# Optimization experiments

Measured on AMD Instinct MI355X. Metric: run time of the kernel, lower is better.

The kernel has to match this reference:

```python
import jax, jax.numpy as jnp
import numpy as np

GAMMA = 2.0  # args.gamma
B, C, H, W = 8, 21, 512, 512


def setup_inputs() -> dict:
    key = jax.random.key(0)
    k1, k2 = jax.random.split(key)
    pred = jax.random.normal(k1, (B, C, H, W), dtype=jnp.float32)
    # one-hot target built from random per-pixel class labels
    labels = jax.random.randint(k2, (B, H, W), 0, C)
    target = jax.nn.one_hot(labels, C, dtype=jnp.float32)  # [B,H,W,C]
    target = jnp.transpose(target, (0, 3, 1, 2))  # [B,C,H,W]
    return {"pred": pred, "target": target}


def reference(pred, target) -> jnp.ndarray:
    b, c, h, w = pred.shape
    logits = jax.nn.log_softmax(pred, axis=1)  # [B,C,H,W]
    lo = jnp.transpose(logits, (0, 2, 3, 1)).reshape(-1, c)  # [N,C]
    tg = jnp.transpose(target, (0, 2, 3, 1)).reshape(-1, c)  # [N,C]
    n = lo.shape[0]
    beta = (n - 1.0) / n
    # per-pixel focal term summed over channels: sum_j (1-p_j)^gamma * log p_j * t_j
    row_val = jnp.sum((1.0 - jnp.exp(lo)) ** GAMMA * lo * tg, axis=1)  # [N]
    mask = (tg == 1).astype(lo.dtype)  # [N,C] class membership mask
    n_c = jnp.sum(mask, axis=0)  # [C] pixels per class
    class_sum = jnp.einsum('nc,n->c', mask, row_val)  # [C] masked reductions
    w = (1.0 - beta) / (1.0 - jnp.power(jnp.float32(beta), n_c) + 1e-6)  # [C]
    return -jnp.sum(w * class_sum) / n
```

## Files before the change

kernel.cpp:

```cpp
#include <hip/hip_runtime.h>

#define CCH    21
#define HWSZ   (512*512)
#define HW4    (HWSZ/4)
#define NPIX   (8*HWSZ)
#define BLKT   256
#define NBLK   (NPIX/4/BLKT)
#define CB     7
#define NB     3

#define WAIT_VM(n) __builtin_amdgcn_s_waitcnt(0x0F70 | (n))

typedef float vfloat4 __attribute__((ext_vector_type(4)));

__device__ __forceinline__ void stage16(const float* g, vfloat4* l) {
    __builtin_amdgcn_global_load_lds(
        (const __attribute__((address_space(1))) unsigned int*)g,
        (__attribute__((address_space(3))) unsigned int*)l, 16, 0, 0);
}

__global__ __launch_bounds__(BLKT) void cb_focal_partial(
    const float* __restrict__ pred, const float* __restrict__ targ,
    float* __restrict__ gsum, float* __restrict__ gcnt)
{
    __shared__ vfloat4 tbuf[2][CB][BLKT];
    __shared__ float ls_sum[CCH];
    __shared__ float ls_cnt[CCH];
    if (threadIdx.x < CCH) { ls_sum[threadIdx.x] = 0.f; ls_cnt[threadIdx.x] = 0.f; }
    __syncthreads();

    const int tid = blockIdx.x * BLKT + threadIdx.x;
    const int b   = tid >> 16;
    const int hw4 = tid & (HW4 - 1);
    const float* pp = pred + (size_t)b * CCH * HWSZ + (size_t)hw4 * 4;
    const float* tp = targ + (size_t)b * CCH * HWSZ + (size_t)hw4 * 4;
    const int wv = threadIdx.x & 192;

    float s0 = 0.f, s1 = 0.f, s2 = 0.f, s3 = 0.f;
    float vy0 = 0.f, vy1 = 0.f, vy2 = 0.f, vy3 = 0.f;
    float ey0 = 1.f, ey1 = 1.f, ey2 = 1.f, ey3 = 1.f;
    int   y0 = 0, y1 = 0, y2 = 0, y3 = 0;

    vfloat4 v[2][CB];

    #pragma unroll
    for (int j = 0; j < CB; ++j)
        stage16(tp + (size_t)j * HWSZ, &tbuf[0][j][wv]);
    #pragma unroll
    for (int j = 0; j < CB; ++j)
        v[0][j] = __builtin_nontemporal_load((const vfloat4*)(pp + (size_t)j * HWSZ));
    __builtin_amdgcn_sched_barrier(0);

    #pragma unroll
    for (int kk = 0; kk < NB; ++kk) {
        if (kk + 1 < NB) {
            #pragma unroll
            for (int j = 0; j < CB; ++j)
                stage16(tp + (size_t)((kk + 1) * CB + j) * HWSZ,
                        &tbuf[(kk + 1) & 1][j][wv]);
            #pragma unroll
            for (int j = 0; j < CB; ++j)
                v[(kk + 1) & 1][j] = __builtin_nontemporal_load(
                    (const vfloat4*)(pp + (size_t)((kk + 1) * CB + j) * HWSZ));
            __builtin_amdgcn_sched_barrier(0);
            WAIT_VM(14);
        } else {
            __builtin_amdgcn_sched_barrier(0);
            WAIT_VM(0);
        }
        __builtin_amdgcn_sched_barrier(0);

        #pragma unroll
        for (int j = 0; j < CB; ++j) {
            const vfloat4 pv = v[kk & 1][j];
            const vfloat4 t  = tbuf[kk & 1][j][threadIdx.x];
            const int c = kk * CB + j;
            const float e0 = __expf(pv.x), e1 = __expf(pv.y),
                        e2 = __expf(pv.z), e3 = __expf(pv.w);
            s0 += e0; s1 += e1; s2 += e2; s3 += e3;
            const bool h0 = t.x > 0.5f, h1 = t.y > 0.5f,
                       h2 = t.z > 0.5f, h3 = t.w > 0.5f;
            y0 = h0 ? c : y0;  vy0 = h0 ? pv.x : vy0;  ey0 = h0 ? e0 : ey0;
            y1 = h1 ? c : y1;  vy1 = h1 ? pv.y : vy1;  ey1 = h1 ? e1 : ey1;
            y2 = h2 ? c : y2;  vy2 = h2 ? pv.z : vy2;  ey2 = h2 ? e2 : ey2;
            y3 = h3 ? c : y3;  vy3 = h3 ? pv.w : vy3;  ey3 = h3 ? e3 : ey3;
        }
    }

    {
        const float l0 = vy0 - __logf(s0), p0 = ey0 / s0, o0 = 1.f - p0;
        const float l1 = vy1 - __logf(s1), p1 = ey1 / s1, o1 = 1.f - p1;
        const float l2 = vy2 - __logf(s2), p2 = ey2 / s2, o2 = 1.f - p2;
        const float l3 = vy3 - __logf(s3), p3 = ey3 / s3, o3 = 1.f - p3;
        atomicAdd(&ls_sum[y0], o0 * o0 * l0);  atomicAdd(&ls_cnt[y0], 1.f);
        atomicAdd(&ls_sum[y1], o1 * o1 * l1);  atomicAdd(&ls_cnt[y1], 1.f);
        atomicAdd(&ls_sum[y2], o2 * o2 * l2);  atomicAdd(&ls_cnt[y2], 1.f);
        atomicAdd(&ls_sum[y3], o3 * o3 * l3);  atomicAdd(&ls_cnt[y3], 1.f);
    }
    __syncthreads();
    if (threadIdx.x < CCH) {
        atomicAdd(&gsum[threadIdx.x], ls_sum[threadIdx.x]);
        atomicAdd(&gcnt[threadIdx.x], ls_cnt[threadIdx.x]);
    }
}

__global__ void cb_focal_final(const float* __restrict__ gsum,
                               const float* __restrict__ gcnt,
                               float* __restrict__ out)
{
    const int lane = threadIdx.x;
    double term = 0.0;
    if (lane < CCH) {
        const double n    = (double)NPIX;
        const double beta = (n - 1.0) / n;
        const double w = (1.0 - beta) / (1.0 - pow(beta, (double)gcnt[lane]) + 1e-6);
        term = w * (double)gsum[lane];
    }
    for (int off = 32; off; off >>= 1) term += __shfl_down(term, off, 64);
    if (lane == 0) out[0] = (float)(-term / (double)NPIX);
}

extern "C" void kernel_launch(void* const* d_in, const int* in_sizes, int n_in,
                              void* d_out, int out_size, void* d_ws, size_t ws_size,
                              hipStream_t stream) {
    const float* pred = (const float*)d_in[0];
    const float* targ = (const float*)d_in[1];
    float* out  = (float*)d_out;
    float* gsum = (float*)d_ws;
    float* gcnt = gsum + CCH;

    (void)hipMemsetAsync(gsum, 0, 2 * CCH * sizeof(float), stream);
    cb_focal_partial<<<NBLK, BLKT, 0, stream>>>(pred, targ, gsum, gcnt);
    cb_focal_final<<<1, 64, 0, stream>>>(gsum, gcnt, out);
}
```

Before: 346.5 us.

## Replace LDS-staged double buffer with per-channel register prefetch ring

Drops the global_load_lds staging of the one-hot target and the 7-channel double-buffered blocks. Both pred and target now load straight into registers through a 4-deep rolling prefetch ring, with explicit vmcnt waits per channel. This frees shared memory and cuts register pressure, which can raise occupancy. In exchange there are fewer bytes in flight per thread, the hand-counted waitcnt values are fragile, and the nontemporal hint on pred loads is removed.

```diff
diff --git a/kernel.cpp b/kernel.cpp
--- a/kernel.cpp
+++ b/kernel.cpp
@@ -6,24 +6,16 @@
 #define NPIX   (8*HWSZ)
 #define BLKT   256
 #define NBLK   (NPIX/4/BLKT)
-#define CB     7
-#define NB     3
+#define PF     4
 
 #define WAIT_VM(n) __builtin_amdgcn_s_waitcnt(0x0F70 | (n))
 
 typedef float vfloat4 __attribute__((ext_vector_type(4)));
 
-__device__ __forceinline__ void stage16(const float* g, vfloat4* l) {
-    __builtin_amdgcn_global_load_lds(
-        (const __attribute__((address_space(1))) unsigned int*)g,
-        (__attribute__((address_space(3))) unsigned int*)l, 16, 0, 0);
-}
-
 __global__ __launch_bounds__(BLKT) void cb_focal_partial(
     const float* __restrict__ pred, const float* __restrict__ targ,
     float* __restrict__ gsum, float* __restrict__ gcnt)
 {
-    __shared__ vfloat4 tbuf[2][CB][BLKT];
     __shared__ float ls_sum[CCH];
     __shared__ float ls_cnt[CCH];
     if (threadIdx.x < CCH) { ls_sum[threadIdx.x] = 0.f; ls_cnt[threadIdx.x] = 0.f; }
@@ -34,57 +26,47 @@
     const int hw4 = tid & (HW4 - 1);
     const float* pp = pred + (size_t)b * CCH * HWSZ + (size_t)hw4 * 4;
     const float* tp = targ + (size_t)b * CCH * HWSZ + (size_t)hw4 * 4;
-    const int wv = threadIdx.x & 192;
 
     float s0 = 0.f, s1 = 0.f, s2 = 0.f, s3 = 0.f;
     float vy0 = 0.f, vy1 = 0.f, vy2 = 0.f, vy3 = 0.f;
     float ey0 = 1.f, ey1 = 1.f, ey2 = 1.f, ey3 = 1.f;
     int   y0 = 0, y1 = 0, y2 = 0, y3 = 0;
 
-    vfloat4 v[2][CB];
+    vfloat4 pv[PF], tv[PF];
 
     #pragma unroll
-    for (int j = 0; j < CB; ++j)
-        stage16(tp + (size_t)j * HWSZ, &tbuf[0][j][wv]);
-    #pragma unroll
-    for (int j = 0; j < CB; ++j)
-        v[0][j] = __builtin_nontemporal_load((const vfloat4*)(pp + (size_t)j * HWSZ));
-    __builtin_amdgcn_sched_barrier(0);
+    for (int c = 0; c < PF; ++c) {
+        pv[c] = *(const vfloat4*)(pp + (size_t)c * HWSZ);
+        tv[c] = *(const vfloat4*)(tp + (size_t)c * HWSZ);
+        __builtin_amdgcn_sched_barrier(0);
+    }
 
     #pragma unroll
-    for (int kk = 0; kk < NB; ++kk) {
-        if (kk + 1 < NB) {
-            #pragma unroll
-            for (int j = 0; j < CB; ++j)
-                stage16(tp + (size_t)((kk + 1) * CB + j) * HWSZ,
-                        &tbuf[(kk + 1) & 1][j][wv]);
-            #pragma unroll
-            for (int j = 0; j < CB; ++j)
-                v[(kk + 1) & 1][j] = __builtin_nontemporal_load(
-                    (const vfloat4*)(pp + (size_t)((kk + 1) * CB + j) * HWSZ));
-            __builtin_amdgcn_sched_barrier(0);
-            WAIT_VM(14);
-        } else {
-            __builtin_amdgcn_sched_barrier(0);
-            WAIT_VM(0);
+    for (int c = 0; c < CCH; ++c) {
+        if      (c <= CCH - 4) { WAIT_VM(6); }
+        else if (c == CCH - 3) { WAIT_VM(4); }
+        else if (c == CCH - 2) { WAIT_VM(2); }
+        else                   { WAIT_VM(0); }
+        __builtin_amdgcn_sched_barrier(0);
+
+        const vfloat4 p = pv[c % PF];
+        const vfloat4 t = tv[c % PF];
+
+        if (c + PF < CCH) {
+            pv[c % PF] = *(const vfloat4*)(pp + (size_t)(c + PF) * HWSZ);
+            tv[c % PF] = *(const vfloat4*)(tp + (size_t)(c + PF) * HWSZ);
         }
         __builtin_amdgcn_sched_barrier(0);
 
-        #pragma unroll
-        for (int j = 0; j < CB; ++j) {
-            const vfloat4 pv = v[kk & 1][j];
-            const vfloat4 t  = tbuf[kk & 1][j][threadIdx.x];
-            const int c = kk * CB + j;
-            const float e0 = __expf(pv.x), e1 = __expf(pv.y),
-                        e2 = __expf(pv.z), e3 = __expf(pv.w);
-            s0 += e0; s1 += e1; s2 += e2; s3 += e3;
-            const bool h0 = t.x > 0.5f, h1 = t.y > 0.5f,
-                       h2 = t.z > 0.5f, h3 = t.w > 0.5f;
-            y0 = h0 ? c : y0;  vy0 = h0 ? pv.x : vy0;  ey0 = h0 ? e0 : ey0;
-            y1 = h1 ? c : y1;  vy1 = h1 ? pv.y : vy1;  ey1 = h1 ? e1 : ey1;
-            y2 = h2 ? c : y2;  vy2 = h2 ? pv.z : vy2;  ey2 = h2 ? e2 : ey2;
-            y3 = h3 ? c : y3;  vy3 = h3 ? pv.w : vy3;  ey3 = h3 ? e3 : ey3;
-        }
+        const float e0 = __expf(p.x), e1 = __expf(p.y),
+                    e2 = __expf(p.z), e3 = __expf(p.w);
+        s0 += e0; s1 += e1; s2 += e2; s3 += e3;
+        const bool h0 = t.x > 0.5f, h1 = t.y > 0.5f,
+                   h2 = t.z > 0.5f, h3 = t.w > 0.5f;
+        y0 = h0 ? c : y0;  vy0 = h0 ? p.x : vy0;  ey0 = h0 ? e0 : ey0;
+        y1 = h1 ? c : y1;  vy1 = h1 ? p.y : vy1;  ey1 = h1 ? e1 : ey1;
+        y2 = h2 ? c : y2;  vy2 = h2 ? p.z : vy2;  ey2 = h2 ? e2 : ey2;
+        y3 = h3 ? c : y3;  vy3 = h3 ? p.w : vy3;  ey3 = h3 ? e3 : ey3;
     }
 
     {
```

Measured after the change: 360.3 us. +4.0%, slower.
